# Kernel tuning notes

Hardware: AMD Instinct MI355X
Metric: run time of the kernel (lower is better)

Reference implementation:

```python
import jax, jax.numpy as jnp
import numpy as np

NUM_HEADS = 16
HEAD_DIM = 128  # embedding_size 2048 / 16 heads
ROPE_BASE = 10000.0


def rope_tables(seq_len, head_dim):
    # matches precompute_rope_params with freq_config=None
    inv_freq = 1.0 / (ROPE_BASE ** (jnp.arange(0, head_dim, 2, dtype=jnp.float32) / head_dim))
    pos = jnp.arange(seq_len, dtype=jnp.float32)
    ang = pos[:, None] * inv_freq[None, :]          # [S, D/2]
    ang = jnp.concatenate([ang, ang], axis=1)        # [S, D]
    return jnp.cos(ang), jnp.sin(ang)


def apply_rope(x, cos, sin):
    # x: [B, H, S, D]
    d = x.shape[-1]
    x1, x2 = x[..., : d // 2], x[..., d // 2:]
    rotated = jnp.concatenate([-x2, x1], axis=-1)
    return x * cos[None, None] + rotated * sin[None, None]


def setup_inputs() -> dict:
    key = jax.random.key(0)
    ks = jax.random.split(key, 5)
    B, S, H = 2, 2048, 2048
    w_scale = 1.0 / np.sqrt(H)  # keep activations sane
    return {
        "x": jax.random.normal(ks[0], (B, S, H), dtype=jnp.float32),
        "Wq": jax.random.normal(ks[1], (H, H), dtype=jnp.float32) * w_scale,
        "Wk": jax.random.normal(ks[2], (H, H), dtype=jnp.float32) * w_scale,
        "Wv": jax.random.normal(ks[3], (H, H), dtype=jnp.float32) * w_scale,
        "Wo": jax.random.normal(ks[4], (H, H), dtype=jnp.float32) * w_scale,
    }


def reference(x, Wq, Wk, Wv, Wo):
    B, S, H = x.shape
    nH, D = NUM_HEADS, HEAD_DIM
    # torch Linear(bias=False): y = x @ W.T
    q = (x @ Wq.T).reshape(B, S, nH, D).transpose(0, 2, 1, 3)  # [B,H,S,D]
    k = (x @ Wk.T).reshape(B, S, nH, D).transpose(0, 2, 1, 3)
    v = (x @ Wv.T).reshape(B, S, nH, D).transpose(0, 2, 1, 3)
    cos, sin = rope_tables(S, D)
    q = apply_rope(q, cos, sin)
    k = apply_rope(k, cos, sin)  # note: v is NOT rotated, matching source
    # Faithful to source bug: scores / (1/sqrt(d)) == scores * sqrt(d)
    scale = jnp.sqrt(jnp.asarray(D, dtype=x.dtype))
    scores = jnp.einsum("bhqd,bhkd->bhqk", q, k) * scale
    causal = jnp.triu(jnp.ones((S, S), dtype=bool), k=1)
    scores = jnp.where(causal[None, None], -jnp.inf, scores)
    attn = jax.nn.softmax(scores, axis=-1)
    ctx = jnp.einsum("bhqk,bhkd->bhqd", attn, v)
    ctx = ctx.transpose(0, 2, 1, 3).reshape(B, S, H)
    return ctx @ Wo.T
```

## Files before the change

### kernel.cpp

```cpp
#include <hip/hip_runtime.h>
#include <cmath>


typedef unsigned short u16;
typedef __attribute__((ext_vector_type(4))) float  f32x4;
typedef __attribute__((ext_vector_type(16))) float f32x16;
typedef __attribute__((ext_vector_type(4))) float  float4v;
typedef __attribute__((ext_vector_type(4))) unsigned short u16x4;
typedef __attribute__((ext_vector_type(8))) unsigned short u16x8;
typedef __attribute__((ext_vector_type(8))) short s16x8;

__device__ __forceinline__ u16 f2bf(float f) {
  unsigned u = __float_as_uint(f);
  u += 0x7FFFu + ((u >> 16) & 1u);
  return (u16)(u >> 16);
}
__device__ __forceinline__ float bf2f(u16 h) {
  return __uint_as_float(((unsigned)h) << 16);
}
__device__ __forceinline__ f32x16 MFMA32(s16x8 a, s16x8 b, f32x16 c) {
  return __builtin_amdgcn_mfma_f32_32x32x16_bf16(a, b, c, 0, 0, 0);
}
__device__ __forceinline__ unsigned cvtpk_bf16(float lo, float hi) {
  unsigned r;
  asm("v_cvt_pk_bf16_f32 %0, %1, %2" : "=v"(r) : "v"(lo), "v"(hi));
  return r;
}
__device__ __forceinline__ void gld16(const void* g, void* s) {
  __builtin_amdgcn_global_load_lds(
      (const __attribute__((address_space(1))) void*)g,
      (__attribute__((address_space(3))) void*)s, 16, 0, 0);
}

__global__ void split_bf16(const float* __restrict__ src, u16* __restrict__ hi,
                           u16* __restrict__ lo, int n4) {
  int i = blockIdx.x * 256 + threadIdx.x;
  if (i >= n4) return;
  float4v v = ((const float4v*)src)[i];
  u16x4 hv, lv;
#pragma unroll
  for (int j = 0; j < 4; ++j) {
    float f = v[j];
    u16 h = f2bf(f);
    hv[j] = h;
    lv[j] = f2bf(f - bf2f(h));
  }
  ((u16x4*)hi)[i] = hv;
  if (lo) ((u16x4*)lo)[i] = lv;
}

__global__ void rope_tab(float* __restrict__ cosT, float* __restrict__ sinT) {
  int idx = blockIdx.x * 256 + threadIdx.x;
  int i = idx & 63, s = idx >> 6;
  double invf = pow(10000.0, -(double)i / 64.0);
  double ang = (double)s * invf;
  cosT[idx] = (float)cos(ang);
  sinT[idx] = (float)sin(ang);
}

__global__ __launch_bounds__(512, 1)
void gemm_qk(const u16* __restrict__ xh, const u16* __restrict__ xl,
             const u16* __restrict__ Wqh, const u16* __restrict__ Wql,
             const u16* __restrict__ Wkh, const u16* __restrict__ Wkl,
             u16* __restrict__ Qh, u16* __restrict__ Ql,
             u16* __restrict__ Kh, u16* __restrict__ Kl,
             const float* __restrict__ cosT, const float* __restrict__ sinT,
             float qscale, int M, int N, int K) {
  __shared__ u16 SM[2 * 32768];
  const int t = threadIdx.x;
  const int w = t >> 6, lane = t & 63;
  const int l31 = lane & 31, hi = lane >> 5;
  const int wm = w >> 1, wn = w & 1;

  const int bid = (int)blockIdx.x + 16 * (int)blockIdx.y;
  const int xcd = bid & 7, slot = bid >> 3;
  const int bn = 2 * xcd + (slot & 1);
  const int bm = slot >> 1;

  const size_t arow0 = (size_t)bm * 256, brow0 = (size_t)bn * 128;

  const int pA0 = 128 * w + lane;
  const int pA1 = pA0 + 64;
  const int pB0 = 64 * w + lane;
  const int qA0 = pA0 ^ ((pA0 >> 3) & 7);
  const int qA1 = pA1 ^ ((pA1 >> 3) & 7);
  const int qB0 = pB0 ^ ((pB0 >> 3) & 7);
  const size_t gA0 = (arow0 + (qA0 >> 2)) * (size_t)K + (qA0 & 3) * 8;
  const size_t gA1 = (arow0 + (qA1 >> 2)) * (size_t)K + (qA1 & 3) * 8;
  const size_t gB0 = (brow0 + (qB0 >> 2)) * (size_t)K + (qB0 & 3) * 8;

  auto stageA = [&](int k0, int bp) {
    u16* P = &SM[bp * 32768];
    gld16(&xh[gA0 + k0], P + 1024 * w);
    gld16(&xh[gA1 + k0], P + 1024 * w + 512);
    gld16(&xl[gA0 + k0], P + 8192 + 1024 * w);
    gld16(&xl[gA1 + k0], P + 8192 + 1024 * w + 512);
  };
  auto stageB = [&](int k0, int bp) {
    u16* P = &SM[bp * 32768];
    gld16(&Wqh[gB0 + k0], P + 16384 + 512 * w);
    gld16(&Wql[gB0 + k0], P + 20480 + 512 * w);
    gld16(&Wkh[gB0 + k0], P + 24576 + 512 * w);
    gld16(&Wkl[gB0 + k0], P + 28672 + 512 * w);
  };

  auto aoff = [&](int fm, int ks) {
    int q = ((64 * wm + 32 * fm + l31) << 2) | (2 * ks + hi);
    q ^= (q >> 3) & 7;
    return q * 8;
  };
  auto boff = [&](int fn, int ks) {
    int q = ((32 * wn + 64 * fn + l31) << 2) | (2 * ks + hi);
    q ^= (q >> 3) & 7;
    return q * 8;
  };

  f32x16 accq[2][2], acck[2][2];
#pragma unroll
  for (int fm = 0; fm < 2; ++fm)
#pragma unroll
    for (int fn = 0; fn < 2; ++fn)
#pragma unroll
      for (int r = 0; r < 16; ++r) { accq[fm][fn][r] = 0.f; acck[fm][fn][r] = 0.f; }

  const int NK = K >> 5;
  stageA(0, 0);
  stageB(0, 0);
  asm volatile("s_waitcnt vmcnt(0)" ::: "memory");
  __builtin_amdgcn_sched_barrier(0);
  __builtin_amdgcn_s_barrier();
  __builtin_amdgcn_sched_barrier(0);

  int bp = 0;
  for (int kt = 0; kt < NK; ++kt) {
    const u16* P = &SM[bp * 32768];
    const bool more = (kt + 1 < NK);

    s16x8 a_h[2][2], a_l[2][2];
    {
      s16x8 bq_h[2][2], bq_l[2][2];
#pragma unroll
      for (int ks = 0; ks < 2; ++ks)
#pragma unroll
        for (int fm = 0; fm < 2; ++fm) {
          a_h[ks][fm] = *(const s16x8*)&P[aoff(fm, ks)];
          a_l[ks][fm] = *(const s16x8*)&P[8192 + aoff(fm, ks)];
        }
#pragma unroll
      for (int ks = 0; ks < 2; ++ks)
#pragma unroll
        for (int fn = 0; fn < 2; ++fn) {
          bq_h[ks][fn] = *(const s16x8*)&P[16384 + boff(fn, ks)];
          bq_l[ks][fn] = *(const s16x8*)&P[20480 + boff(fn, ks)];
        }
      if (more) stageA((kt + 1) * 32, bp ^ 1);
      __builtin_amdgcn_sched_barrier(0);
      __builtin_amdgcn_s_barrier();
      asm volatile("s_waitcnt lgkmcnt(0)" ::: "memory");
      __builtin_amdgcn_sched_barrier(0);
      __builtin_amdgcn_s_setprio(1);
#pragma unroll
      for (int ks = 0; ks < 2; ++ks)
#pragma unroll
        for (int fm = 0; fm < 2; ++fm)
#pragma unroll
          for (int fn = 0; fn < 2; ++fn) {
            accq[fm][fn] = MFMA32(a_h[ks][fm], bq_h[ks][fn], accq[fm][fn]);
            accq[fm][fn] = MFMA32(a_h[ks][fm], bq_l[ks][fn], accq[fm][fn]);
            accq[fm][fn] = MFMA32(a_l[ks][fm], bq_h[ks][fn], accq[fm][fn]);
          }
      __builtin_amdgcn_s_setprio(0);
      __builtin_amdgcn_sched_barrier(0);
      __builtin_amdgcn_s_barrier();
      __builtin_amdgcn_sched_barrier(0);
    }

    {
      s16x8 bk_h[2][2], bk_l[2][2];
#pragma unroll
      for (int ks = 0; ks < 2; ++ks)
#pragma unroll
        for (int fn = 0; fn < 2; ++fn) {
          bk_h[ks][fn] = *(const s16x8*)&P[24576 + boff(fn, ks)];
          bk_l[ks][fn] = *(const s16x8*)&P[28672 + boff(fn, ks)];
        }
      if (more) stageB((kt + 1) * 32, bp ^ 1);
      __builtin_amdgcn_sched_barrier(0);
      __builtin_amdgcn_s_barrier();
      asm volatile("s_waitcnt lgkmcnt(0)" ::: "memory");
      __builtin_amdgcn_sched_barrier(0);
      __builtin_amdgcn_s_setprio(1);
#pragma unroll
      for (int ks = 0; ks < 2; ++ks)
#pragma unroll
        for (int fm = 0; fm < 2; ++fm)
#pragma unroll
          for (int fn = 0; fn < 2; ++fn) {
            acck[fm][fn] = MFMA32(a_h[ks][fm], bk_h[ks][fn], acck[fm][fn]);
            acck[fm][fn] = MFMA32(a_h[ks][fm], bk_l[ks][fn], acck[fm][fn]);
            acck[fm][fn] = MFMA32(a_l[ks][fm], bk_h[ks][fn], acck[fm][fn]);
          }
      __builtin_amdgcn_s_setprio(0);
      __builtin_amdgcn_sched_barrier(0);
      asm volatile("s_waitcnt vmcnt(0)" ::: "memory");
      __builtin_amdgcn_s_barrier();
      __builtin_amdgcn_sched_barrier(0);
    }
    bp ^= 1;
  }

  const int hd = 32 * wn + l31;
#pragma unroll
  for (int fm = 0; fm < 2; ++fm)
#pragma unroll
    for (int r = 0; r < 16; ++r) {
      const int row = bm * 256 + 64 * wm + 32 * fm + (r & 3) + 8 * (r >> 2) + 4 * hi;
      const int s = row & 2047;
      const float cs = cosT[s * 64 + hd], sn = sinT[s * 64 + hd];
      const size_t p1 = (size_t)row * N + bn * 128 + hd;
      {
        const float q1 = accq[fm][0][r], q2 = accq[fm][1][r];
        const float o1 = (q1 * cs - q2 * sn) * qscale;
        const float o2 = (q2 * cs + q1 * sn) * qscale;
        const u16 h1 = f2bf(o1);
        Qh[p1] = h1; Ql[p1] = f2bf(o1 - bf2f(h1));
        const u16 h2 = f2bf(o2);
        Qh[p1 + 64] = h2; Ql[p1 + 64] = f2bf(o2 - bf2f(h2));
      }
      {
        const float k1 = acck[fm][0][r], k2 = acck[fm][1][r];
        const float o1 = k1 * cs - k2 * sn;
        const float o2 = k2 * cs + k1 * sn;
        const u16 h1 = f2bf(o1);
        Kh[p1] = h1; Kl[p1] = f2bf(o1 - bf2f(h1));
        const u16 h2 = f2bf(o2);
        Kh[p1 + 64] = h2; Kl[p1 + 64] = f2bf(o2 - bf2f(h2));
      }
    }
}

template <int NTERM, int OMODE, int ROPE, int GX>
__global__ __launch_bounds__(512, NTERM == 3 ? 1 : 4)
void gemm8(const u16* __restrict__ Ah, const u16* __restrict__ Al,
           const u16* __restrict__ Bh, const u16* __restrict__ Bl,
           float* __restrict__ Cf, u16* __restrict__ Ch, u16* __restrict__ Cl,
           const float* __restrict__ cosT, const float* __restrict__ sinT,
           float scale, int M, int N, int K) {
  constexpr int BUF = (NTERM == 3) ? 24576 : 12288;
  constexpr int BHI = (NTERM == 3) ? 16384 : 8192;
  constexpr int PER = GX / 8;
  constexpr int PSH = (PER == 2) ? 1 : 2;
  static_assert(PER == 2 || PER == 4, "grid.x must be 16 or 32");
  __shared__ u16 SM[3 * BUF];
  const int t = threadIdx.x;
  const int w = t >> 6, lane = t & 63;
  const int l31 = lane & 31, hi = lane >> 5;
  const int wm = w >> 1, wn = w & 1;

  const int bid = (int)blockIdx.x + GX * (int)blockIdx.y;
  const int xcd = bid & 7, slot = bid >> 3;
  const int bn = PER * xcd + (slot & (PER - 1));
  const int bm = slot >> PSH;

  const size_t arow0 = (size_t)bm * 256, brow0 = (size_t)bn * 128;

  const int pA0 = 128 * w + lane;
  const int pA1 = pA0 + 64;
  const int pB0 = 64 * w + lane;
  const int qA0 = pA0 ^ ((pA0 >> 3) & 7);
  const int qA1 = pA1 ^ ((pA1 >> 3) & 7);
  const int qB0 = pB0 ^ ((pB0 >> 3) & 7);
  const size_t gA0 = (arow0 + (qA0 >> 2)) * (size_t)K + (qA0 & 3) * 8;
  const size_t gA1 = (arow0 + (qA1 >> 2)) * (size_t)K + (qA1 & 3) * 8;
  const size_t gB0 = (brow0 + (qB0 >> 2)) * (size_t)K + (qB0 & 3) * 8;

  auto stage = [&](int k0, int bp) {
    u16* P = &SM[bp * BUF];
    gld16(&Ah[gA0 + k0], P + 1024 * w);
    gld16(&Ah[gA1 + k0], P + 1024 * w + 512);
    gld16(&Bh[gB0 + k0], P + BHI + 512 * w);
    if constexpr (NTERM == 3) {
      gld16(&Al[gA0 + k0], P + 8192 + 1024 * w);
      gld16(&Al[gA1 + k0], P + 8192 + 1024 * w + 512);
      gld16(&Bl[gB0 + k0], P + BHI + 4096 + 512 * w);
    }
  };

  auto aoff = [&](int fm, int ks) {
    int q = ((64 * wm + 32 * fm + l31) << 2) | (2 * ks + hi);
    q ^= (q >> 3) & 7;
    return q * 8;
  };
  auto boff = [&](int fn, int ks) {
    int q = ((32 * wn + 64 * fn + l31) << 2) | (2 * ks + hi);
    q ^= (q >> 3) & 7;
    return q * 8;
  };

  f32x16 acc[2][2];
#pragma unroll
  for (int fm = 0; fm < 2; ++fm)
#pragma unroll
    for (int fn = 0; fn < 2; ++fn)
#pragma unroll
      for (int r = 0; r < 16; ++r) acc[fm][fn][r] = 0.f;

  const int NK = K >> 5;
  stage(0, 0);
  if (NK > 1) stage(32, 1);
  int cur = 0, nxt = 1, fut = 2;
  for (int kt = 0; kt < NK; ++kt) {
    if (kt + 2 < NK) {
      stage((kt + 2) * 32, fut);
      if constexpr (NTERM == 3)
        asm volatile("s_waitcnt vmcnt(12)" ::: "memory");
      else
        asm volatile("s_waitcnt vmcnt(6)" ::: "memory");
    } else if (kt + 1 < NK) {
      if constexpr (NTERM == 3)
        asm volatile("s_waitcnt vmcnt(6)" ::: "memory");
      else
        asm volatile("s_waitcnt vmcnt(3)" ::: "memory");
    } else {
      asm volatile("s_waitcnt vmcnt(0)" ::: "memory");
    }
    __builtin_amdgcn_sched_barrier(0);
    __builtin_amdgcn_s_barrier();
    __builtin_amdgcn_sched_barrier(0);

    const u16* P = &SM[cur * BUF];
    __builtin_amdgcn_s_setprio(1);
#pragma unroll
    for (int ks = 0; ks < 2; ++ks) {
      s16x8 a_h[2], a_l[2], b_h[2], b_l[2];
#pragma unroll
      for (int fm = 0; fm < 2; ++fm) {
        a_h[fm] = *(const s16x8*)&P[aoff(fm, ks)];
        if constexpr (NTERM == 3)
          a_l[fm] = *(const s16x8*)&P[8192 + aoff(fm, ks)];
      }
#pragma unroll
      for (int fn = 0; fn < 2; ++fn) {
        b_h[fn] = *(const s16x8*)&P[BHI + boff(fn, ks)];
        if constexpr (NTERM == 3)
          b_l[fn] = *(const s16x8*)&P[BHI + 4096 + boff(fn, ks)];
      }
#pragma unroll
      for (int fm = 0; fm < 2; ++fm)
#pragma unroll
        for (int fn = 0; fn < 2; ++fn) {
          acc[fm][fn] = MFMA32(a_h[fm], b_h[fn], acc[fm][fn]);
          if constexpr (NTERM == 3) {
            acc[fm][fn] = MFMA32(a_h[fm], b_l[fn], acc[fm][fn]);
            acc[fm][fn] = MFMA32(a_l[fm], b_h[fn], acc[fm][fn]);
          }
        }
    }
    __builtin_amdgcn_s_setprio(0);
    __builtin_amdgcn_s_barrier();
    const int tmp = cur; cur = nxt; nxt = fut; fut = tmp;
  }

  if constexpr (ROPE) {
    const int hd = 32 * wn + l31;
#pragma unroll
    for (int fm = 0; fm < 2; ++fm)
#pragma unroll
      for (int r = 0; r < 16; ++r) {
        const int row = bm * 256 + 64 * wm + 32 * fm + (r & 3) + 8 * (r >> 2) + 4 * hi;
        const int s = row & 2047;
        const float cs = cosT[s * 64 + hd], sn = sinT[s * 64 + hd];
        const float q1 = acc[fm][0][r], q2 = acc[fm][1][r];
        const float o1 = (q1 * cs - q2 * sn) * scale;
        const float o2 = (q2 * cs + q1 * sn) * scale;
        const size_t p1 = (size_t)row * N + bn * 128 + hd;
        const u16 h1 = f2bf(o1);
        Ch[p1] = h1; Cl[p1] = f2bf(o1 - bf2f(h1));
        const u16 h2 = f2bf(o2);
        Ch[p1 + 64] = h2; Cl[p1 + 64] = f2bf(o2 - bf2f(h2));
      }
  } else {
#pragma unroll
    for (int fm = 0; fm < 2; ++fm)
#pragma unroll
      for (int fn = 0; fn < 2; ++fn)
#pragma unroll
        for (int r = 0; r < 16; ++r) {
          const int row = bm * 256 + 64 * wm + 32 * fm + (r & 3) + 8 * (r >> 2) + 4 * hi;
          const int col = bn * 128 + 32 * wn + 64 * fn + l31;
          const float v = acc[fm][fn][r];
          if constexpr (OMODE == 0) {
            Cf[(size_t)row * N + col] = v;
          } else if constexpr (OMODE == 1) {
            const u16 hv = f2bf(v);
            Ch[(size_t)row * N + col] = hv;
            Cl[(size_t)row * N + col] = f2bf(v - bf2f(hv));
          } else {
            Ch[(size_t)row * N + col] = f2bf(v);
          }
        }
  }
}

__global__ __launch_bounds__(512, 2)
void attn(const u16* __restrict__ Qh, const u16* __restrict__ Ql,
          const u16* __restrict__ Kh, const u16* __restrict__ Kl,
          const u16* __restrict__ Vt, u16* __restrict__ Ctx) {
  __shared__ u16 SMEM[65536];

  const int t = threadIdx.x;
  const int w = t >> 6, lane = t & 63;
  const int l31 = lane & 31, hi = lane >> 5;
  const int swz = (l31 & 7) << 3;
  const int j = w >> 1, kh = w & 1;

  const int bid = (int)blockIdx.x + 8 * (int)blockIdx.y + 128 * (int)blockIdx.z;
  const int xcd = bid & 7, slot = bid >> 3;
  const int h = xcd * 2 + (slot >> 4);
  const int rem = slot & 15;
  const int qtA = rem & 7, bA = rem >> 3;

  const int offK0 = (8 * w + (lane >> 4)) * 2048 + (((lane & 15) ^ ((lane >> 4) & 7)) * 8);
  const int offK1 = (8 * w + 4 + (lane >> 4)) * 2048 + (((lane & 15) ^ ((4 + (lane >> 4)) & 7)) * 8);
  const int offV0 = (16 * w + (lane >> 3)) * 4096 + (((lane & 7) ^ ((lane >> 3) & 7)) * 8);
  const int offV1 = offV0 + 8 * 4096;

  auto stage = [&](const u16* gK, const u16* gKlo, const u16* gV, int kt, int bp) {
    u16* B = &SMEM[bp * 24576];
    const int ka = kt * 131072;
    const int va = kt * 64;
    gld16(gK + ka + offK0, B + 1024 * w);
    gld16(gK + ka + offK1, B + 1024 * w + 512);
    gld16(gKlo + ka + offK0, B + 8192 + 1024 * w);
    gld16(gKlo + ka + offK1, B + 8192 + 1024 * w + 512);
    gld16(gV + va + offV0, B + 16384 + 1024 * w);
    gld16(gV + va + offV1, B + 16384 + 1024 * w + 512);
  };

  int bufph = 0;
  {
    const u16* gK0 = Kh + ((size_t)(bA * 2048)) * 2048 + h * 128;
    const u16* gL0 = Kl + ((size_t)(bA * 2048)) * 2048 + h * 128;
    const u16* gV0 = Vt + (size_t)(h * 128) * 4096 + bA * 2048;
    stage(gK0, gL0, gV0, 0, 0);
  }

  for (int task = 0; task < 2; ++task) {
    const int qt = task ? 15 - qtA : qtA;
    const int bb = task ? 1 - bA : bA;
    const u16* gK0 = Kh + ((size_t)(bb * 2048)) * 2048 + h * 128;
    const u16* gL0 = Kl + ((size_t)(bb * 2048)) * 2048 + h * 128;
    const u16* gV0 = Vt + (size_t)(h * 128) * 4096 + bb * 2048;
    const int nb = 1 - bb;
    const u16* nK0 = Kh + ((size_t)(nb * 2048)) * 2048 + h * 128;
    const u16* nL0 = Kl + ((size_t)(nb * 2048)) * 2048 + h * 128;
    const u16* nV0 = Vt + (size_t)(h * 128) * 4096 + nb * 2048;

    const int q0 = qt * 128 + 32 * j;
    const int qg = q0 + l31;
    s16x8 qfh[8], qfl[8];
    {
      const size_t qbase = ((size_t)(bb * 2048 + qg)) * 2048 + h * 128 + 8 * hi;
#pragma unroll
      for (int s = 0; s < 8; ++s) {
        qfh[s] = *(const s16x8*)&Qh[qbase + 16 * s];
        qfl[s] = *(const s16x8*)&Ql[qbase + 16 * s];
      }
    }

    float m_run = -3.0e38f, l_run = 0.f;
    f32x16 o[4];
#pragma unroll
    for (int d = 0; d < 4; ++d)
#pragma unroll
      for (int r = 0; r < 16; ++r) o[d][r] = 0.f;

    const int nt = 2 * qt + 2;
    for (int kt = 0; kt < nt; ++kt) {
      bool staged = true;
      if (kt + 1 < nt)      stage(gK0, gL0, gV0, kt + 1, bufph ^ 1);
      else if (task == 0)   stage(nK0, nL0, nV0, 0, bufph ^ 1);
      else                  staged = false;
      if (staged) asm volatile("s_waitcnt vmcnt(6)" ::: "memory");
      else        asm volatile("s_waitcnt vmcnt(0)" ::: "memory");
      __builtin_amdgcn_sched_barrier(0);
      __builtin_amdgcn_s_barrier();
      __builtin_amdgcn_sched_barrier(0);

      const int kb0 = kt * 64 + 32 * kh;
      const bool active = (q0 + 31) >= kb0;
      if (active) {
        const u16* Kb = &SMEM[bufph * 24576];
        const u16* Lb = Kb + 8192;
        const u16* Vb = Kb + 16384;
        f32x16 acc;
#pragma unroll
        for (int r = 0; r < 16; ++r) acc[r] = 0.f;
        __builtin_amdgcn_s_setprio(1);
#pragma unroll
        for (int s = 0; s < 8; ++s) {
          const int col = 16 * s + 8 * hi;
          const s16x8 kha = *(const s16x8*)&Kb[((32 * kh + l31) * 128 + col) ^ swz];
          const s16x8 kla = *(const s16x8*)&Lb[((32 * kh + l31) * 128 + col) ^ swz];
          acc = MFMA32(kha, qfh[s], acc);
          acc = MFMA32(kla, qfh[s], acc);
          acc = MFMA32(kha, qfl[s], acc);
        }
        __builtin_amdgcn_s_setprio(0);

        const bool partial = (kb0 + 31) > q0;
        float mx = -3.0e38f;
#pragma unroll
        for (int r = 0; r < 16; ++r) {
          const int koff = (r & 3) + 8 * (r >> 2) + 4 * hi;
          float v = acc[r];
          if (partial && (kb0 + koff > qg)) v = -3.0e38f;
          acc[r] = v;
          mx = fmaxf(mx, v);
        }
        mx = fmaxf(mx, __shfl_xor(mx, 32));
        const float mn = fmaxf(m_run, mx);
        const float al = __expf(m_run - mn);
        m_run = mn;
        float rs = 0.f;
#pragma unroll
        for (int r = 0; r < 16; ++r) {
          const float e = __expf(acc[r] - mn);
          acc[r] = e;
          rs += e;
        }
        rs += __shfl_xor(rs, 32);
        l_run = l_run * al + rs;
#pragma unroll
        for (int d = 0; d < 4; ++d)
#pragma unroll
          for (int r = 0; r < 16; ++r) o[d][r] *= al;

        s16x8 pb[2];
#pragma unroll
        for (int tt = 0; tt < 2; ++tt) {
          const int q2A = 2 * tt;
          const float e0 = acc[4 * q2A + 0], e1 = acc[4 * q2A + 1];
          const float e2 = acc[4 * q2A + 2], e3 = acc[4 * q2A + 3];
          const float f0 = acc[4 * q2A + 4], f1 = acc[4 * q2A + 5];
          const float f2 = acc[4 * q2A + 6], f3 = acc[4 * q2A + 7];
          unsigned a0 = cvtpk_bf16(e0, e1);
          unsigned a1 = cvtpk_bf16(e2, e3);
          unsigned b0 = cvtpk_bf16(f0, f1);
          unsigned b1 = cvtpk_bf16(f2, f3);
          asm volatile("v_permlane32_swap_b32 %0, %1" : "+v"(a0), "+v"(b0));
          asm volatile("v_permlane32_swap_b32 %0, %1" : "+v"(a1), "+v"(b1));
          union { unsigned u[4]; s16x8 v; } pk;
          pk.u[0] = a0; pk.u[1] = a1; pk.u[2] = b0; pk.u[3] = b1;
          pb[tt] = pk.v;
        }

        __builtin_amdgcn_s_setprio(1);
#pragma unroll
        for (int d = 0; d < 4; ++d) {
#pragma unroll
          for (int tt = 0; tt < 2; ++tt) {
            const s16x8 va = *(const s16x8*)
                &Vb[((32 * d + l31) * 64 + 16 * (2 * kh + tt) + 8 * hi) ^ swz];
            o[d] = MFMA32(va, pb[tt], o[d]);
          }
        }
        __builtin_amdgcn_s_setprio(0);
      }
      __builtin_amdgcn_s_barrier();
      bufph ^= 1;
    }

    float* Sf = (float*)&SMEM[49152];
    Sf[w * 64 + lane] = m_run;
    Sf[512 + w * 64 + lane] = l_run;
    asm volatile("s_waitcnt lgkmcnt(0)" ::: "memory");
    __builtin_amdgcn_s_barrier();
    const float mOth = Sf[(w ^ 1) * 64 + lane];
    const float lOth = Sf[512 + (w ^ 1) * 64 + lane];
    const float mC = fmaxf(m_run, mOth);
    const float eS = __expf(m_run - mC);
    const float eO = __expf(mOth - mC);
    const float lC = eS * l_run + eO * lOth;
#pragma unroll
    for (int d = 0; d < 4; ++d)
#pragma unroll
      for (int r = 0; r < 16; ++r) o[d][r] *= eS;
    __builtin_amdgcn_s_barrier();
#pragma unroll
    for (int round = 0; round < 2; ++round) {
      if ((w >> 2) == round && kh == 1) {
        const int sl = j & 1;
#pragma unroll
        for (int d = 0; d < 4; ++d)
#pragma unroll
          for (int rr = 0; rr < 4; ++rr) {
            float4v c;
            c[0] = o[d][4 * rr + 0]; c[1] = o[d][4 * rr + 1];
            c[2] = o[d][4 * rr + 2]; c[3] = o[d][4 * rr + 3];
            const int cidx = 4 * (d * 4 + rr);
            *(float4v*)&Sf[sl * 4096 + ((lane * 64 + cidx) ^ ((lane & 7) << 2))] = c;
          }
      }
      asm volatile("s_waitcnt lgkmcnt(0)" ::: "memory");
      __builtin_amdgcn_s_barrier();
      if ((w >> 2) == round && kh == 0) {
        const int sl = j & 1;
#pragma unroll
        for (int d = 0; d < 4; ++d)
#pragma unroll
          for (int rr = 0; rr < 4; ++rr) {
            const int cidx = 4 * (d * 4 + rr);
            const float4v c =
                *(const float4v*)&Sf[sl * 4096 + ((lane * 64 + cidx) ^ ((lane & 7) << 2))];
            o[d][4 * rr + 0] += c[0]; o[d][4 * rr + 1] += c[1];
            o[d][4 * rr + 2] += c[2]; o[d][4 * rr + 3] += c[3];
          }
      }
      __builtin_amdgcn_s_barrier();
    }
    u16* Os = &SMEM[49152];
    if (kh == 0) {
      const float inv_l = 1.0f / lC;
      const int rl = 32 * j + l31;
#pragma unroll
      for (int d = 0; d < 4; ++d)
#pragma unroll
        for (int r = 0; r < 16; r += 2) {
          const int dd = 32 * d + (r & 3) + 8 * (r >> 2) + 4 * hi;
          const unsigned pr = cvtpk_bf16(o[d][r] * inv_l, o[d][r + 1] * inv_l);
          *(unsigned*)&Os[(rl * 128 + dd) ^ ((rl & 7) << 3)] = pr;
        }
    }
    asm volatile("s_waitcnt lgkmcnt(0)" ::: "memory");
    __builtin_amdgcn_s_barrier();
    {
      const int rr = t >> 2, cb = (t & 3) * 32;
      const size_t ob =
          ((size_t)(bb * 2048 + qt * 128 + rr)) * 2048 + h * 128 + cb;
#pragma unroll
      for (int p = 0; p < 4; ++p)
        *(u16x8*)&Ctx[ob + 8 * p] =
            *(const u16x8*)&Os[(rr * 128 + cb + 8 * p) ^ ((rr & 7) << 3)];
    }
    asm volatile("s_waitcnt lgkmcnt(0)" ::: "memory");
    __builtin_amdgcn_s_barrier();
  }
}

extern "C" void kernel_launch(void* const* d_in, const int* in_sizes, int n_in,
                              void* d_out, int out_size, void* d_ws, size_t ws_size,
                              hipStream_t stream) {
  const float* x  = (const float*)d_in[0];
  const float* Wq = (const float*)d_in[1];
  const float* Wk = (const float*)d_in[2];
  const float* Wv = (const float*)d_in[3];
  const float* Wo = (const float*)d_in[4];
  float* out = (float*)d_out;

  char* ws = (char*)d_ws;
  size_t off = 0;
  auto alloc = [&](size_t bytes) {
    char* p = ws + off;
    off += (bytes + 255) & ~(size_t)255;
    return p;
  };
  const size_t XE = (size_t)4096 * 2048;
  const size_t WE = (size_t)2048 * 2048;

  u16* xh  = (u16*)alloc(XE * 2);
  u16* xl  = (u16*)alloc(XE * 2);
  u16* Wqh = (u16*)alloc(WE * 2);
  u16* Wql = (u16*)alloc(WE * 2);
  u16* Wkh = (u16*)alloc(WE * 2);
  u16* Wkl = (u16*)alloc(WE * 2);
  u16* Wvh = (u16*)alloc(WE * 2);
  u16* Woh = (u16*)alloc(WE * 2);
  u16* Qhb = (u16*)alloc(XE * 2);
  u16* Qlb = (u16*)alloc(XE * 2);
  u16* Khb = (u16*)alloc(XE * 2);
  u16* Klb = (u16*)alloc(XE * 2);
  u16* Vtb = (u16*)alloc(XE * 2);
  u16* Ctxb = (u16*)alloc(XE * 2);
  float* cosT = (float*)alloc((size_t)2048 * 64 * 4);
  float* sinT = (float*)alloc((size_t)2048 * 64 * 4);
  (void)ws_size;
  (void)in_sizes; (void)n_in; (void)out_size;

  split_bf16<<<8192, 256, 0, stream>>>(x, xh, xl, (int)(XE / 4));
  split_bf16<<<4096, 256, 0, stream>>>(Wq, Wqh, Wql, (int)(WE / 4));
  split_bf16<<<4096, 256, 0, stream>>>(Wk, Wkh, Wkl, (int)(WE / 4));
  split_bf16<<<4096, 256, 0, stream>>>(Wv, Wvh, nullptr, (int)(WE / 4));
  split_bf16<<<4096, 256, 0, stream>>>(Wo, Woh, nullptr, (int)(WE / 4));
  rope_tab<<<512, 256, 0, stream>>>(cosT, sinT);

  gemm_qk<<<dim3(16, 16), 512, 0, stream>>>(
      xh, xl, Wqh, Wql, Wkh, Wkl, Qhb, Qlb, Khb, Klb, cosT, sinT,
      11.313708498984760f, 4096, 2048, 2048);
  gemm8<1, 2, 0, 32><<<dim3(32, 8), 512, 0, stream>>>(
      Wvh, nullptr, xh, nullptr, nullptr, Vtb, nullptr, nullptr, nullptr,
      1.0f, 2048, 4096, 2048);

  attn<<<dim3(8, 16, 2), 512, 0, stream>>>(Qhb, Qlb, Khb, Klb, Vtb, Ctxb);

  gemm8<1, 0, 0, 16><<<dim3(16, 16), 512, 0, stream>>>(
      Ctxb, nullptr, Woh, nullptr, out, nullptr, nullptr, nullptr, nullptr,
      1.0f, 4096, 2048, 2048);
}
```

Baseline: 519.8 us.

## Merge split kernels and deepen K-tile to 64 with double buffering in 1-term GEMMs

The five bf16 split launches become one 2D-grid kernel, which removes launch overhead. The single-term GEMM (V projection and output projection) is specialized into gemm1k. It uses a K-step of 64 instead of 32 and two LDS buffers instead of three, so each barrier covers twice the MFMA work. The LDS footprint grows, and launch bounds drop to one block per CU, which may reduce latency hiding across blocks.

Measured after the change: 501.2 us. 3.6% less time.

```diff
diff --git a/kernel.cpp b/kernel.cpp
--- a/kernel.cpp
+++ b/kernel.cpp
@@ -32,10 +32,22 @@
       (__attribute__((address_space(3))) void*)s, 16, 0, 0);
 }
 
-__global__ void split_bf16(const float* __restrict__ src, u16* __restrict__ hi,
-                           u16* __restrict__ lo, int n4) {
-  int i = blockIdx.x * 256 + threadIdx.x;
-  if (i >= n4) return;
+__global__ void split_all(const float* __restrict__ x, const float* __restrict__ Wq,
+                          const float* __restrict__ Wk, const float* __restrict__ Wv,
+                          const float* __restrict__ Wo,
+                          u16* __restrict__ xh, u16* __restrict__ xl,
+                          u16* __restrict__ Wqh, u16* __restrict__ Wql,
+                          u16* __restrict__ Wkh, u16* __restrict__ Wkl,
+                          u16* __restrict__ Wvh, u16* __restrict__ Woh) {
+  const int y = blockIdx.y;
+  const int base = blockIdx.x * 256 + threadIdx.x;
+  const float* src; u16* dh; u16* dl = nullptr; int i = base;
+  if (y == 0)      { src = x;  dh = xh;  dl = xl; }
+  else if (y == 1) { src = x;  dh = xh;  dl = xl; i = base + (1 << 20); }
+  else if (y == 2) { src = Wq; dh = Wqh; dl = Wql; }
+  else if (y == 3) { src = Wk; dh = Wkh; dl = Wkl; }
+  else if (y == 4) { src = Wv; dh = Wvh; }
+  else             { src = Wo; dh = Woh; }
   float4v v = ((const float4v*)src)[i];
   u16x4 hv, lv;
 #pragma unroll
@@ -45,8 +57,8 @@
     hv[j] = h;
     lv[j] = f2bf(f - bf2f(h));
   }
-  ((u16x4*)hi)[i] = hv;
-  if (lo) ((u16x4*)lo)[i] = lv;
+  ((u16x4*)dh)[i] = hv;
+  if (dl) ((u16x4*)dl)[i] = lv;
 }
 
 __global__ void rope_tab(float* __restrict__ cosT, float* __restrict__ sinT) {
@@ -239,19 +251,15 @@
     }
 }
 
-template <int NTERM, int OMODE, int ROPE, int GX>
-__global__ __launch_bounds__(512, NTERM == 3 ? 1 : 4)
-void gemm8(const u16* __restrict__ Ah, const u16* __restrict__ Al,
-           const u16* __restrict__ Bh, const u16* __restrict__ Bl,
-           float* __restrict__ Cf, u16* __restrict__ Ch, u16* __restrict__ Cl,
-           const float* __restrict__ cosT, const float* __restrict__ sinT,
-           float scale, int M, int N, int K) {
-  constexpr int BUF = (NTERM == 3) ? 24576 : 12288;
-  constexpr int BHI = (NTERM == 3) ? 16384 : 8192;
+template <int OMODE, int GX>
+__global__ __launch_bounds__(512, 1)
+void gemm1k(const u16* __restrict__ Ah, const u16* __restrict__ Bh,
+            float* __restrict__ Cf, u16* __restrict__ Ch,
+            int M, int N, int K) {
   constexpr int PER = GX / 8;
   constexpr int PSH = (PER == 2) ? 1 : 2;
   static_assert(PER == 2 || PER == 4, "grid.x must be 16 or 32");
-  __shared__ u16 SM[3 * BUF];
+  __shared__ u16 SM[2 * 24576];
   const int t = threadIdx.x;
   const int w = t >> 6, lane = t & 63;
   const int l31 = lane & 31, hi = lane >> 5;
@@ -261,40 +269,40 @@
   const int xcd = bid & 7, slot = bid >> 3;
   const int bn = PER * xcd + (slot & (PER - 1));
   const int bm = slot >> PSH;
-
   const size_t arow0 = (size_t)bm * 256, brow0 = (size_t)bn * 128;
 
-  const int pA0 = 128 * w + lane;
-  const int pA1 = pA0 + 64;
-  const int pB0 = 64 * w + lane;
-  const int qA0 = pA0 ^ ((pA0 >> 3) & 7);
-  const int qA1 = pA1 ^ ((pA1 >> 3) & 7);
-  const int qB0 = pB0 ^ ((pB0 >> 3) & 7);
-  const size_t gA0 = (arow0 + (qA0 >> 2)) * (size_t)K + (qA0 & 3) * 8;
-  const size_t gA1 = (arow0 + (qA1 >> 2)) * (size_t)K + (qA1 & 3) * 8;
-  const size_t gB0 = (brow0 + (qB0 >> 2)) * (size_t)K + (qB0 & 3) * 8;
+  size_t gA[4], gB[2];
+#pragma unroll
+  for (int i = 0; i < 4; ++i) {
+    const int p = 512 * i + 64 * w + lane;
+    const int q = p ^ ((p >> 3) & 7);
+    gA[i] = (arow0 + (q >> 3)) * (size_t)K + (q & 7) * 8;
+  }
+#pragma unroll
+  for (int i = 0; i < 2; ++i) {
+    const int p = 512 * i + 64 * w + lane;
+    const int q = p ^ ((p >> 3) & 7);
+    gB[i] = (brow0 + (q >> 3)) * (size_t)K + (q & 7) * 8;
+  }
 
   auto stage = [&](int k0, int bp) {
-    u16* P = &SM[bp * BUF];
-    gld16(&Ah[gA0 + k0], P + 1024 * w);
-    gld16(&Ah[gA1 + k0], P + 1024 * w + 512);
-    gld16(&Bh[gB0 + k0], P + BHI + 512 * w);
-    if constexpr (NTERM == 3) {
-      gld16(&Al[gA0 + k0], P + 8192 + 1024 * w);
-      gld16(&Al[gA1 + k0], P + 8192 + 1024 * w + 512);
-      gld16(&Bl[gB0 + k0], P + BHI + 4096 + 512 * w);
-    }
-  };
-
+    u16* P = &SM[bp * 24576];
+#pragma unroll
+    for (int i = 0; i < 4; ++i)
+      gld16(&Ah[gA[i] + k0], P + 4096 * i + 512 * w);
+#pragma unroll
+    for (int i = 0; i < 2; ++i)
+      gld16(&Bh[gB[i] + k0], P + 16384 + 4096 * i + 512 * w);
+  };
   auto aoff = [&](int fm, int ks) {
-    int q = ((64 * wm + 32 * fm + l31) << 2) | (2 * ks + hi);
-    q ^= (q >> 3) & 7;
-    return q * 8;
+    int g = ((64 * wm + 32 * fm + l31) << 3) | (2 * ks + hi);
+    g ^= (g >> 3) & 7;
+    return g * 8;
   };
   auto boff = [&](int fn, int ks) {
-    int q = ((32 * wn + 64 * fn + l31) << 2) | (2 * ks + hi);
-    q ^= (q >> 3) & 7;
-    return q * 8;
+    int g = ((32 * wn + 64 * fn + l31) << 3) | (2 * ks + hi);
+    g ^= (g >> 3) & 7;
+    return 16384 + g * 8;
   };
 
   f32x16 acc[2][2];
@@ -305,22 +313,13 @@
 #pragma unroll
       for (int r = 0; r < 16; ++r) acc[fm][fn][r] = 0.f;
 
-  const int NK = K >> 5;
+  const int NK = K >> 6;
   stage(0, 0);
-  if (NK > 1) stage(32, 1);
-  int cur = 0, nxt = 1, fut = 2;
+  int bp = 0;
   for (int kt = 0; kt < NK; ++kt) {
-    if (kt + 2 < NK) {
-      stage((kt + 2) * 32, fut);
-      if constexpr (NTERM == 3)
-        asm volatile("s_waitcnt vmcnt(12)" ::: "memory");
-      else
-        asm volatile("s_waitcnt vmcnt(6)" ::: "memory");
-    } else if (kt + 1 < NK) {
-      if constexpr (NTERM == 3)
-        asm volatile("s_waitcnt vmcnt(6)" ::: "memory");
-      else
-        asm volatile("s_waitcnt vmcnt(3)" ::: "memory");
+    if (kt + 1 < NK) {
+      stage((kt + 1) * 64, bp ^ 1);
+      asm volatile("s_waitcnt vmcnt(6)" ::: "memory");
     } else {
       asm volatile("s_waitcnt vmcnt(0)" ::: "memory");
     }
@@ -328,78 +327,41 @@
     __builtin_amdgcn_s_barrier();
     __builtin_amdgcn_sched_barrier(0);
 
-    const u16* P = &SM[cur * BUF];
+    const u16* P = &SM[bp * 24576];
     __builtin_amdgcn_s_setprio(1);
 #pragma unroll
-    for (int ks = 0; ks < 2; ++ks) {
-      s16x8 a_h[2], a_l[2], b_h[2], b_l[2];
-#pragma unroll
-      for (int fm = 0; fm < 2; ++fm) {
-        a_h[fm] = *(const s16x8*)&P[aoff(fm, ks)];
-        if constexpr (NTERM == 3)
-          a_l[fm] = *(const s16x8*)&P[8192 + aoff(fm, ks)];
-      }
-#pragma unroll
-      for (int fn = 0; fn < 2; ++fn) {
-        b_h[fn] = *(const s16x8*)&P[BHI + boff(fn, ks)];
-        if constexpr (NTERM == 3)
-          b_l[fn] = *(const s16x8*)&P[BHI + 4096 + boff(fn, ks)];
-      }
+    for (int ks = 0; ks < 4; ++ks) {
+      s16x8 a_h[2], b_h[2];
+#pragma unroll
+      for (int fm = 0; fm < 2; ++fm) a_h[fm] = *(const s16x8*)&P[aoff(fm, ks)];
+#pragma unroll
+      for (int fn = 0; fn < 2; ++fn) b_h[fn] = *(const s16x8*)&P[boff(fn, ks)];
 #pragma unroll
       for (int fm = 0; fm < 2; ++fm)
 #pragma unroll
-        for (int fn = 0; fn < 2; ++fn) {
+        for (int fn = 0; fn < 2; ++fn)
           acc[fm][fn] = MFMA32(a_h[fm], b_h[fn], acc[fm][fn]);
-          if constexpr (NTERM == 3) {
-            acc[fm][fn] = MFMA32(a_h[fm], b_l[fn], acc[fm][fn]);
-            acc[fm][fn] = MFMA32(a_l[fm], b_h[fn], acc[fm][fn]);
-          }
-        }
     }
     __builtin_amdgcn_s_setprio(0);
     __builtin_amdgcn_s_barrier();
-    const int tmp = cur; cur = nxt; nxt = fut; fut = tmp;
+    bp ^= 1;
   }
 
-  if constexpr (ROPE) {
-    const int hd = 32 * wn + l31;
-#pragma unroll
-    for (int fm = 0; fm < 2; ++fm)
+#pragma unroll
+  for (int fm = 0; fm < 2; ++fm)
+#pragma unroll
+    for (int fn = 0; fn < 2; ++fn)
 #pragma unroll
       for (int r = 0; r < 16; ++r) {
         const int row = bm * 256 + 64 * wm + 32 * fm + (r & 3) + 8 * (r >> 2) + 4 * hi;
-        const int s = row & 2047;
-        const float cs = cosT[s * 64 + hd], sn = sinT[s * 64 + hd];
-        const float q1 = acc[fm][0][r], q2 = acc[fm][1][r];
-        const float o1 = (q1 * cs - q2 * sn) * scale;
-        const float o2 = (q2 * cs + q1 * sn) * scale;
-        const size_t p1 = (size_t)row * N + bn * 128 + hd;
-        const u16 h1 = f2bf(o1);
-        Ch[p1] = h1; Cl[p1] = f2bf(o1 - bf2f(h1));
-        const u16 h2 = f2bf(o2);
-        Ch[p1 + 64] = h2; Cl[p1 + 64] = f2bf(o2 - bf2f(h2));
+        const int col = bn * 128 + 32 * wn + 64 * fn + l31;
+        const float v = acc[fm][fn][r];
+        if constexpr (OMODE == 0) {
+          Cf[(size_t)row * N + col] = v;
+        } else {
+          Ch[(size_t)row * N + col] = f2bf(v);
+        }
       }
-  } else {
-#pragma unroll
-    for (int fm = 0; fm < 2; ++fm)
-#pragma unroll
-      for (int fn = 0; fn < 2; ++fn)
-#pragma unroll
-        for (int r = 0; r < 16; ++r) {
-          const int row = bm * 256 + 64 * wm + 32 * fm + (r & 3) + 8 * (r >> 2) + 4 * hi;
-          const int col = bn * 128 + 32 * wn + 64 * fn + l31;
-          const float v = acc[fm][fn][r];
-          if constexpr (OMODE == 0) {
-            Cf[(size_t)row * N + col] = v;
-          } else if constexpr (OMODE == 1) {
-            const u16 hv = f2bf(v);
-            Ch[(size_t)row * N + col] = hv;
-            Cl[(size_t)row * N + col] = f2bf(v - bf2f(hv));
-          } else {
-            Ch[(size_t)row * N + col] = f2bf(v);
-          }
-        }
-  }
 }
 
 __global__ __launch_bounds__(512, 2)
@@ -687,23 +649,18 @@
   (void)ws_size;
   (void)in_sizes; (void)n_in; (void)out_size;
 
-  split_bf16<<<8192, 256, 0, stream>>>(x, xh, xl, (int)(XE / 4));
-  split_bf16<<<4096, 256, 0, stream>>>(Wq, Wqh, Wql, (int)(WE / 4));
-  split_bf16<<<4096, 256, 0, stream>>>(Wk, Wkh, Wkl, (int)(WE / 4));
-  split_bf16<<<4096, 256, 0, stream>>>(Wv, Wvh, nullptr, (int)(WE / 4));
-  split_bf16<<<4096, 256, 0, stream>>>(Wo, Woh, nullptr, (int)(WE / 4));
+  split_all<<<dim3(4096, 6), 256, 0, stream>>>(
+      x, Wq, Wk, Wv, Wo, xh, xl, Wqh, Wql, Wkh, Wkl, Wvh, Woh);
   rope_tab<<<512, 256, 0, stream>>>(cosT, sinT);
 
   gemm_qk<<<dim3(16, 16), 512, 0, stream>>>(
       xh, xl, Wqh, Wql, Wkh, Wkl, Qhb, Qlb, Khb, Klb, cosT, sinT,
       11.313708498984760f, 4096, 2048, 2048);
-  gemm8<1, 2, 0, 32><<<dim3(32, 8), 512, 0, stream>>>(
-      Wvh, nullptr, xh, nullptr, nullptr, Vtb, nullptr, nullptr, nullptr,
-      1.0f, 2048, 4096, 2048);
+  gemm1k<2, 32><<<dim3(32, 8), 512, 0, stream>>>(
+      Wvh, xh, nullptr, Vtb, 2048, 4096, 2048);
 
   attn<<<dim3(8, 16, 2), 512, 0, stream>>>(Qhb, Qlb, Khb, Klb, Vtb, Ctxb);
 
-  gemm8<1, 0, 0, 16><<<dim3(16, 16), 512, 0, stream>>>(
-      Ctxb, nullptr, Woh, nullptr, out, nullptr, nullptr, nullptr, nullptr,
-      1.0f, 4096, 2048, 2048);
-}
+  gemm1k<0, 16><<<dim3(16, 16), 512, 0, stream>>>(
+      Ctxb, Woh, out, nullptr, 4096, 2048, 2048);
+}
```
